# Optimization experiments

Measured on AMD Instinct MI355X. Metric: run time of the kernel, lower is better.

The kernel has to match this reference:

```python
import jax, jax.numpy as jnp
import numpy as np

# ---- static config (mirrors GaussianLSS __init__) ----
ORF_H, ORF_W = 256, 704
FC, FH, FW = 128, 32, 88
D_ST, D_END, D_STEP = 4.0, 45.0, 1.0
OUT_C = 128
ERROR_TOL = 1.0
OPACITY_THR = 0.05
XB = (-50.0, 50.0, 1.0)
YB = (-50.0, 50.0, 1.0)
BEV_H = int(round((YB[1] - YB[0]) / YB[2]))
BEV_W = int(round((XB[1] - XB[0]) / XB[2]))
DS = np.arange(D_ST, D_END, D_STEP, dtype=np.float32)
D = DS.shape[0]  # 41
BN_EPS = 1e-3
CHUNK = 512      # gaussians composited per scan step (16896 = 33*512)
B, NCAM = 1, 6


def make_frustum():
    ds = jnp.broadcast_to(jnp.asarray(DS)[:, None, None], (D, FH, FW))
    xs = jnp.broadcast_to(jnp.linspace(0.0, ORF_W - 1.0, FW)[None, None, :], (D, FH, FW))
    ys = jnp.broadcast_to(jnp.linspace(0.0, ORF_H - 1.0, FH)[None, :, None], (D, FH, FW))
    return jnp.stack([xs, ys, ds], -1)  # [D,FH,FW,3]


def get_geometry(rots, trans, intrins, post_rots, post_trans):
    fr = make_frustum()
    pts = fr[None, None] - post_trans[:, :, None, None, None, :]
    pts = jnp.einsum('bnij,bndhwj->bndhwi', jnp.linalg.inv(post_rots), pts)
    pts = jnp.concatenate([pts[..., :2] * pts[..., 2:3], pts[..., 2:3]], -1)
    comb = jnp.einsum('bnij,bnjk->bnik', rots, jnp.linalg.inv(intrins))
    pts = jnp.einsum('bnij,bndhwj->bndhwi', comb, pts) + trans[:, :, None, None, None, :]
    return pts  # [B,N,D,FH,FW,3] ego-frame frustum points


def conv2d(x, w, b, pad):
    y = jax.lax.conv_general_dilated(x, w, (1, 1), [(pad, pad), (pad, pad)],
                                     dimension_numbers=('NCHW', 'OIHW', 'NCHW'))
    return y + b[None, :, None, None]


def bnorm(x, g, bt, m, v):
    s = (g / jnp.sqrt(v + BN_EPS))[None, :, None, None]
    return (x - m[None, :, None, None]) * s + bt[None, :, None, None]


def splat(means, cov6, colors, ops, valid_in):
    # Differentiable BEV gaussian rasterization (3DGS math, orthographic BEV camera,
    # all depths equal -> compositing in stable gaussian-index order).
    H, W = BEV_H, BEV_W
    sh, sw = H / 2.0, W / 2.0  # h/h_meters with FoV=2 (BEVCamera)
    my = -sh * means[:, 1] + H / 2.0  # pixel row (full_proj_transform row 0)
    mx = -sw * means[:, 0] + W / 2.0  # pixel col (row 1)
    a = sh * sh * cov6[:, 3] + 0.3    # 2D cov = J Sigma_xy J^T, +0.3 low-pass as in 3DGS
    c = sw * sw * cov6[:, 0] + 0.3
    b = sh * sw * cov6[:, 1]
    det = a * c - b * b
    valid = valid_in & (det > 0)
    inv_det = jnp.where(det > 0, 1.0 / det, 0.0)
    cA, cB, cC = c * inv_det, -b * inv_det, a * inv_det
    pi = jnp.repeat(jnp.arange(H, dtype=jnp.float32), W)  # [P] pixel rows
    pj = jnp.tile(jnp.arange(W, dtype=jnp.float32), H)    # [P] pixel cols
    G = means.shape[0]
    nchunk = G // CHUNK
    resh = lambda x: x.reshape((nchunk, CHUNK) + x.shape[1:])
    chunks = (resh(my), resh(mx), resh(cA), resh(cB), resh(cC),
              resh(ops), resh(valid), resh(colors))

    def body(carry, ch):
        logT, acc = carry
        my_c, mx_c, A, Bc, Cc, op_c, val_c, col_c = ch
        dI = pi[None, :] - my_c[:, None]                     # [Gc,P]
        dJ = pj[None, :] - mx_c[:, None]
        q = A[:, None] * dI * dI + 2.0 * Bc[:, None] * dI * dJ + Cc[:, None] * dJ * dJ
        alpha = jnp.minimum(0.99, op_c[:, None] * jnp.exp(-0.5 * q))
        alpha = jnp.where(val_c[:, None] & (q >= 0) & (alpha >= 1.0 / 255.0), alpha, 0.0)
        log1m = jnp.log1p(-alpha)
        cum = jnp.cumsum(log1m, axis=0)
        T = jnp.exp(logT[None, :] + cum - log1m)             # transmittance before each gaussian
        acc = acc + jnp.einsum('gp,gc->pc', alpha * T, col_c)
        return (logT + cum[-1], acc), None

    P = H * W
    init = (jnp.zeros((P,), jnp.float32), jnp.zeros((P, colors.shape[1]), jnp.float32))
    (_, acc), _ = jax.lax.scan(jax.checkpoint(body), init, chunks)
    return acc.reshape(H, W, -1).transpose(2, 0, 1)  # [C,H,W], bg is zeros


def _forward(cam2ego_rot, cam2ego_trans, cam_intrins, post_cam2ego_rot, post_cam2ego_trans,
             img_feats, conv1_w, conv1_b, bn1_g, bn1_b, bn1_m, bn1_v,
             conv2_w, conv2_b, bn2_g, bn2_b, bn2_m, bn2_v, conv3_w, conv3_b):
    geom = get_geometry(cam2ego_rot, cam2ego_trans, cam_intrins, post_cam2ego_rot, post_cam2ego_trans)
    b, n = img_feats.shape[:2]
    x = img_feats.reshape(b * n, FC, FH, FW)
    x = jax.nn.relu(bnorm(conv2d(x, conv1_w, conv1_b, 1), bn1_g, bn1_b, bn1_m, bn1_v))
    x = jax.nn.relu(bnorm(conv2d(x, conv2_w, conv2_b, 1), bn2_g, bn2_b, bn2_m, bn2_v))
    x = conv2d(x, conv3_w, conv3_b, 0)
    depth_prob = jax.nn.softmax(x[:, :D], axis=1).reshape(b, n, D, FH, FW)
    opac = jax.nn.sigmoid(x[:, D:D + 1]).reshape(b, n, FH, FW)
    feats = x[:, D + 1:].reshape(b, n, OUT_C, FH, FW)
    # per-pixel gaussian moments of the depth distribution (compute_gaussian)
    means = jnp.einsum('bndhw,bndhwi->bnhwi', depth_prob, geom)
    delta = means[:, :, None] - geom                                       # [B,N,D,FH,FW,3]
    cov = jnp.einsum('bndhw,bndhwi,bndhwj->bnhwij', depth_prob, delta, delta) * (ERROR_TOL ** 2 / 9.0)
    center = jnp.array([(XB[0] + XB[1]) / 2.0, (YB[0] + YB[1]) / 2.0, 0.0], jnp.float32)
    scale = jnp.array([2.0 / (XB[1] - XB[0]), 2.0 / (YB[1] - YB[0]), 1.0], jnp.float32)
    m_n = (means - center) * scale
    cov_n = cov * (scale[:, None] * scale[None, :])
    cov6 = jnp.stack([cov_n[..., 0, 0], cov_n[..., 0, 1], cov_n[..., 0, 2],
                      cov_n[..., 1, 1], cov_n[..., 1, 2], cov_n[..., 2, 2]], -1)
    g = n * FH * FW
    colors = feats.transpose(0, 1, 3, 4, 2).reshape(b, g, OUT_C)
    m_n = m_n.reshape(b, g, 3)
    cov6 = cov6.reshape(b, g, 6)
    ops = opac.reshape(b, g)
    mask = ops > OPACITY_THR  # opacity filtering == zero contribution, order preserved
    bev = jax.vmap(splat)(m_n, cov6, colors, ops, mask)                    # [B,C,H,W]
    num_gaussians = mask.astype(jnp.float32).sum(-1).mean()
    return bev, num_gaussians


def setup_inputs():
    key = jax.random.key(0)
    ks = jax.random.split(key, 8)
    # camera-to-ego rotations: cam->ego axis permutation composed with per-camera yaw
    yaw = np.linspace(0.0, 2.0 * np.pi, NCAM, endpoint=False).astype(np.float32)
    cz, sz = np.cos(yaw), np.sin(yaw)
    rotz = np.zeros((NCAM, 3, 3), np.float32)
    rotz[:, 0, 0] = cz; rotz[:, 0, 1] = -sz
    rotz[:, 1, 0] = sz; rotz[:, 1, 1] = cz
    rotz[:, 2, 2] = 1.0
    perm = np.array([[0.0, 0.0, 1.0], [-1.0, 0.0, 0.0], [0.0, -1.0, 0.0]], np.float32)
    rots = np.einsum('nij,jk->nik', rotz, perm)
    cam2ego_rot = jnp.asarray(np.broadcast_to(rots, (B, NCAM, 3, 3)).copy())
    cam2ego_trans = jax.random.normal(ks[0], (B, NCAM, 3), jnp.float32)
    K = np.array([[600.0, 0.0, ORF_W / 2.0], [0.0, 600.0, ORF_H / 2.0], [0.0, 0.0, 1.0]], np.float32)
    cam_intrins = jnp.asarray(np.broadcast_to(K, (B, NCAM, 3, 3)).copy())
    post_cam2ego_rot = jnp.broadcast_to(jnp.eye(3, dtype=jnp.float32), (B, NCAM, 3, 3)) + jnp.zeros((B, NCAM, 3, 3), jnp.float32)
    post_cam2ego_trans = jnp.zeros((B, NCAM, 3), jnp.float32)
    img_feats = jax.random.normal(ks[1], (B, NCAM, FC, FH, FW), jnp.float32)
    def conv_init(k, o, i, kh, kw):
        return jax.random.normal(k, (o, i, kh, kw), jnp.float32) * (1.0 / np.sqrt(i * kh * kw))
    return dict(cam2ego_rot=cam2ego_rot, cam2ego_trans=cam2ego_trans, cam_intrins=cam_intrins,
                post_cam2ego_rot=post_cam2ego_rot, post_cam2ego_trans=post_cam2ego_trans,
                img_feats=img_feats,
                conv1_w=conv_init(ks[2], FC, FC, 3, 3), conv1_b=jnp.zeros((FC,), jnp.float32),
                bn1_g=jnp.ones((FC,), jnp.float32), bn1_b=jnp.zeros((FC,), jnp.float32),
                bn1_m=jnp.zeros((FC,), jnp.float32), bn1_v=jnp.ones((FC,), jnp.float32),
                conv2_w=conv_init(ks[3], FC, FC, 3, 3), conv2_b=jnp.zeros((FC,), jnp.float32),
                bn2_g=jnp.ones((FC,), jnp.float32), bn2_b=jnp.zeros((FC,), jnp.float32),
                bn2_m=jnp.zeros((FC,), jnp.float32), bn2_v=jnp.ones((FC,), jnp.float32),
                conv3_w=conv_init(ks[4], OUT_C + D + 1, FC, 1, 1),
                conv3_b=jax.random.normal(ks[5], (OUT_C + D + 1,), jnp.float32) * 0.1)


def reference(cam2ego_rot, cam2ego_trans, cam_intrins, post_cam2ego_rot, post_cam2ego_trans,
              img_feats, conv1_w, conv1_b, bn1_g, bn1_b, bn1_m, bn1_v,
              conv2_w, conv2_b, bn2_g, bn2_b, bn2_m, bn2_v, conv3_w, conv3_b):
    return _forward(cam2ego_rot, cam2ego_trans, cam_intrins, post_cam2ego_rot, post_cam2ego_trans,
                    img_feats, conv1_w, conv1_b, bn1_g, bn1_b, bn1_m, bn1_v,
                    conv2_w, conv2_b, bn2_g, bn2_b, bn2_m, bn2_v, conv3_w, conv3_b)
```

## Files before the change

### kernel.cpp

```cpp
#include <hip/hip_runtime.h>

#define NCAM 6
#define FC   128
#define FH_  32
#define FW_  88
#define NPIX (FH_*FW_)
#define PH   34
#define PW   92
#define PPIX (PH*PW)
#define ND   41
#define X3D  42
#define OUTC 128
#define GTOT (NCAM*NPIX)
#define BEVH 100
#define BEVW 100
#define NPXB (BEVH*BEVW)
#define NTILE 25
#define NWORD 264
#define NMASKW (NTILE*NTILE*NWORD)
#define WCAP  70000
#define CSIZE 64
#define CBLK  2048

#define SZA     (NCAM*FC*PPIX)
#define WS_CAM  0
#define WS_A    256
#define WS_RB   (WS_A  + SZA)
#define WS_X3   (WS_RB + SZA)
#define WS_GS   (WS_X3 + NCAM*X3D*NPIX)
#define WS_WL   (WS_GS + GTOT*8)
#define WS_BASE (WS_WL + WCAP)

__device__ inline void inv3x3(const float* m, float* o) {
    float a=m[0],b=m[1],c=m[2],d=m[3],e=m[4],f=m[5],g=m[6],h=m[7],i=m[8];
    float A=e*i-f*h, B=c*h-b*i, C=b*f-c*e;
    float Dd=f*g-d*i, E=a*i-c*g, F=c*d-a*f;
    float Gg=d*h-e*g, H=b*g-a*h, I=a*e-b*d;
    float r = 1.0f/(a*A + b*Dd + c*Gg);
    o[0]=A*r; o[1]=B*r; o[2]=C*r; o[3]=Dd*r; o[4]=E*r; o[5]=F*r;
    o[6]=Gg*r; o[7]=H*r; o[8]=I*r;
}

__global__ __launch_bounds__(256) void pad_input_kernel(const float* __restrict__ src,
        float* __restrict__ dst, float* __restrict__ rb,
        float* __restrict__ outp, unsigned long long* __restrict__ masks) {
    int idx = blockIdx.x*256 + threadIdx.x;
    if (idx < NMASKW) masks[idx] = 0ull;
    if (idx <= NPXB*OUTC) outp[idx] = 0.0f;
    if (idx >= NCAM*FC*PPIX) return;
    int plane = idx / PPIX, pp = idx - plane*PPIX;
    int y = pp / PW, x = pp - y*PW;
    bool interior = (y >= 1 && y <= FH_ && x >= 1 && x <= FW_);
    float v = 0.0f;
    if (interior)
        v = src[(size_t)plane*NPIX + (y-1)*FW_ + (x-1)];
    dst[idx] = v;
    if (!interior) rb[idx] = 0.0f;
}

__global__ __launch_bounds__(128) void conv3x3_pf_kernel(
        const float* __restrict__ in, float* __restrict__ out, const float* __restrict__ w,
        const float* __restrict__ cb, const float* __restrict__ bg, const float* __restrict__ bb,
        const float* __restrict__ bm, const float* __restrict__ bv) {
    const int n   = blockIdx.x;
    const int co0 = blockIdx.y * 4;
    const int qid = blockIdx.z * 128 + threadIdx.x;
    if (qid >= 704) return;
    const int y = qid / 22, x0 = (qid - y*22) * 4;
    float scale[4], shift[4];
    #pragma unroll
    for (int c=0;c<4;c++) {
        float s = bg[co0+c] * rsqrtf(bv[co0+c] + 1e-3f);
        scale[c] = s;
        shift[c] = (cb[co0+c] - bm[co0+c]) * s + bb[co0+c];
    }
    float acc[4][4] = {};
    const float* ip = in + (size_t)n*FC*PPIX + y*PW + x0;
    const float* wb = w + (size_t)co0*FC*9;
    float4 p4[3]; float2 p2[3];
    #pragma unroll
    for (int r=0;r<3;r++) {
        p4[r] = *(const float4*)(ip + r*PW);
        p2[r] = *(const float2*)(ip + r*PW + 4);
    }
    for (int ci=0; ci<FC; ++ci) {
        float v[3][6];
        #pragma unroll
        for (int r=0;r<3;r++) {
            v[r][0]=p4[r].x; v[r][1]=p4[r].y; v[r][2]=p4[r].z; v[r][3]=p4[r].w;
            v[r][4]=p2[r].x; v[r][5]=p2[r].y;
        }
        if (ci + 1 < FC) {
            const float* ipn = ip + PPIX;
            #pragma unroll
            for (int r=0;r<3;r++) {
                p4[r] = *(const float4*)(ipn + r*PW);
                p2[r] = *(const float2*)(ipn + r*PW + 4);
            }
        }
        #pragma unroll
        for (int c=0;c<4;c++) {
            const float* wr = wb + (size_t)c*FC*9 + ci*9;
            float w00=wr[0],w01=wr[1],w02=wr[2],w10=wr[3],w11=wr[4],
                  w12=wr[5],w20=wr[6],w21=wr[7],w22=wr[8];
            #pragma unroll
            for (int p=0;p<4;p++) {
                float a = acc[c][p];
                a = fmaf(w00, v[0][p], a); a = fmaf(w01, v[0][p+1], a); a = fmaf(w02, v[0][p+2], a);
                a = fmaf(w10, v[1][p], a); a = fmaf(w11, v[1][p+1], a); a = fmaf(w12, v[1][p+2], a);
                a = fmaf(w20, v[2][p], a); a = fmaf(w21, v[2][p+1], a); a = fmaf(w22, v[2][p+2], a);
                acc[c][p] = a;
            }
        }
        ip += PPIX;
    }
    const int po = (y+1)*PW + (x0+1);
    #pragma unroll
    for (int c=0;c<4;c++) {
        float* op = out + ((size_t)n*FC + co0 + c)*PPIX + po;
        #pragma unroll
        for (int p=0;p<4;p++)
            op[p] = fmaxf(fmaf(acc[c][p], scale[c], shift[c]), 0.0f);
    }
}

__global__ __launch_bounds__(256) void conv1x1_kernel(const float* __restrict__ in,
        float* __restrict__ x3d, float* __restrict__ colors,
        const float* __restrict__ w, const float* __restrict__ b) {
    const int n   = blockIdx.x;
    const int px  = blockIdx.y * 256 + threadIdx.x;
    const int co0 = blockIdx.z * 8;
    const int y   = px / FW_, x = px - y*FW_;
    const int pp  = (y+1)*PW + (x+1);
    const float* wr[8];
    float acc[8];
    #pragma unroll
    for (int k=0;k<8;k++) {
        int co = min(co0 + k, 169);
        wr[k]  = w + (size_t)co*FC;
        acc[k] = b[co];
    }
    const float* ip = in + (size_t)n*FC*PPIX + pp;
    #pragma unroll 4
    for (int ci=0; ci<FC; ++ci) {
        float v = ip[(size_t)ci*PPIX];
        #pragma unroll
        for (int k=0;k<8;k++) acc[k] = fmaf(wr[k][ci], v, acc[k]);
    }
    #pragma unroll
    for (int k=0;k<8;k++) {
        int co = co0 + k;
        if (co < X3D)
            x3d[((size_t)n*X3D + co)*NPIX + px] = acc[k];
        else if (co < 170)
            colors[(((size_t)(n*NPIX + px)) << 7) + (co - X3D)] = acc[k];
    }
}

__global__ __launch_bounds__(256) void moments_masks_kernel(const float* __restrict__ x3,
        const float* __restrict__ rot, const float* __restrict__ tr,
        const float* __restrict__ intr, const float* __restrict__ prot,
        const float* __restrict__ ptr_, float* __restrict__ gauss,
        unsigned long long* __restrict__ masks, float* __restrict__ ng) {
    __shared__ float cc[24];
    const int n = blockIdx.x / 11;
    if (threadIdx.x == 0) {
        float M1[9], Ki[9];
        inv3x3(prot + n*9, M1);
        inv3x3(intr + n*9, Ki);
        const float* R = rot + n*9;
        #pragma unroll
        for (int i=0;i<9;i++) cc[i] = M1[i];
        #pragma unroll
        for (int i=0;i<3;i++) cc[9+i] = ptr_[n*3+i];
        #pragma unroll
        for (int i=0;i<3;i++)
            #pragma unroll
            for (int j=0;j<3;j++)
                cc[12+i*3+j] = R[i*3+0]*Ki[0+j] + R[i*3+1]*Ki[3+j] + R[i*3+2]*Ki[6+j];
        #pragma unroll
        for (int i=0;i<3;i++) cc[21+i] = tr[n*3+i];
    }
    __syncthreads();
    const int gi = blockIdx.x*256 + threadIdx.x;
    const int p  = gi - n*NPIX;
    const int h  = p / FW_, xp = p - h*FW_;
    float u = xp * (703.0f/87.0f);
    float v = h  * (255.0f/31.0f);
    float fx = u - cc[9], fy = v - cc[10], fz = -cc[11];
    float p0x = cc[0]*fx + cc[1]*fy + cc[2]*fz;
    float p0y = cc[3]*fx + cc[4]*fy + cc[5]*fz;
    float p0z = cc[6]*fx + cc[7]*fy + cc[8]*fz;
    const float* lg = x3 + (size_t)n*X3D*NPIX + p;

    float lgv[ND];
    #pragma unroll
    for (int d=0; d<ND; ++d) lgv[d] = lg[(size_t)d*NPIX];

    float mxl = -1e30f;
    #pragma unroll
    for (int d=0; d<ND; ++d) mxl = fmaxf(mxl, lgv[d]);

    float s=0.f, sgx=0.f, sgy=0.f;
    #pragma unroll
    for (int d=0; d<ND; ++d) {
        float e  = __expf(lgv[d] - mxl);
        lgv[d] = e;
        float dz = 4.0f + (float)d;
        float pz = p0z + dz*cc[8];
        float px = (p0x + dz*cc[2]) * pz;
        float py = (p0y + dz*cc[5]) * pz;
        float gx = cc[12]*px + cc[13]*py + cc[14]*pz + cc[21];
        float gy = cc[15]*px + cc[16]*py + cc[17]*pz + cc[22];
        s += e; sgx += e*gx; sgy += e*gy;
    }
    float inv_s = 1.0f/s;
    float mex = sgx*inv_s, mey = sgy*inv_s;
    float cxx=0.f, cxy=0.f, cyy=0.f;
    #pragma unroll
    for (int d=0; d<ND; ++d) {
        float e  = lgv[d];
        float dz = 4.0f + (float)d;
        float pz = p0z + dz*cc[8];
        float px = (p0x + dz*cc[2]) * pz;
        float py = (p0y + dz*cc[5]) * pz;
        float gx = cc[12]*px + cc[13]*py + cc[14]*pz + cc[21];
        float gy = cc[15]*px + cc[16]*py + cc[17]*pz + cc[22];
        float dxv = gx - mex, dyv = gy - mey;
        cxx += e*dxv*dxv; cxy += e*dxv*dyv; cyy += e*dyv*dyv;
    }
    const float k9 = inv_s * (1.0f/9.0f);
    cxx *= k9; cxy *= k9; cyy *= k9;

    float lo = lg[(size_t)ND*NPIX];
    float op = 1.0f/(1.0f + __expf(-lo));
    bool mask = op > 0.05f;

    const float SC = 0.02f, SH = 50.0f, SW = 50.0f;
    float my = -SH*(mey*SC) + 50.0f;
    float mx = -SW*(mex*SC) + 50.0f;
    float a  = SH*SH*(cyy*SC*SC) + 0.3f;
    float b  = SH*SW*(cxy*SC*SC);
    float c  = SW*SW*(cxx*SC*SC) + 0.3f;
    float det = a*c - b*b;
    bool valid = mask && (det > 0.0f);
    float A, B2, C, qm, ri, rj;
    if (valid) {
        float idet = 1.0f/det;
        A = c*idet; B2 = -2.0f*b*idet; C = a*idet;
        qm = 2.0f*__logf(255.0f*op);
        ri = sqrtf(qm*a); rj = sqrtf(qm*c);
    } else { A=B2=C=0.f; qm=-1.0f; ri=-1e30f; rj=-1e30f; }
    float* gp = gauss + (size_t)gi*8;
    gp[0]=my; gp[1]=mx; gp[2]=A; gp[3]=B2; gp[4]=C; gp[5]=qm; gp[6]=ri; gp[7]=rj;

    unsigned long long bal = __ballot(mask);
    if ((threadIdx.x & 63) == 0) atomicAdd(ng, (float)__popcll(bal));

    if (!valid) return;
    const float B = 0.5f*B2;
    const float invC = 1.0f / C;
    const float k2 = C*A - B*B;
    int ti0 = max(0, (int)floorf((my - ri) * 0.25f));
    int ti1 = min(NTILE-1, (int)floorf((my + ri) * 0.25f));
    const int wi = gi >> 6;
    const unsigned long long bit = 1ull << (gi & 63);
    for (int ti = ti0; ti <= ti1; ++ti) {
        float jmn = 1e30f, jmx = -1e30f;
        #pragma unroll
        for (int r = 0; r < 4; ++r) {
            int i = 4*ti + r;
            if (i < 0 || i > 99) continue;
            float di = (float)i - my;
            float disc = C*qm - k2*di*di;
            if (disc < 0.0f) continue;
            float sd = sqrtf(disc);
            float jc = -B*di;
            jmn = fminf(jmn, (jc - sd)*invC + mx);
            jmx = fmaxf(jmx, (jc + sd)*invC + mx);
        }
        if (jmx < jmn) continue;
        int jl = max(0, (int)ceilf(jmn));
        int jh = min(99, (int)floorf(jmx));
        if (jl > jh) continue;
        for (int tj = (jl >> 2); tj <= (jh >> 2); ++tj)
            atomicOr(&masks[(size_t)(ti*NTILE + tj)*NWORD + wi], bit);
    }
}

__global__ __launch_bounds__(256) void cnt_kernel(const unsigned long long* __restrict__ masks,
                                                  int* __restrict__ cnt) {
    __shared__ int sc;
    const int tile = blockIdx.x, t = threadIdx.x;
    if (t == 0) sc = 0;
    __syncthreads();
    if (t < NWORD) atomicAdd(&sc, __popcll(masks[(size_t)tile*NWORD + t]));
    __syncthreads();
    if (t == 0) cnt[tile] = sc;
}

__global__ __launch_bounds__(640) void scan_kernel(const int* __restrict__ cnt,
        int* __restrict__ off, int* __restrict__ choff, int* __restrict__ nwork) {
    __shared__ int wsum[16], wsum2[16];
    const int t = threadIdx.x;
    const int lane = t & 63, wv = t >> 6;
    int c  = (t < NTILE*NTILE) ? cnt[t] : 0;
    int ch = (c + CSIZE-1) >> 6;
    int v = c, v2 = ch;
    #pragma unroll
    for (int o = 1; o < 64; o <<= 1) {
        int u  = __shfl_up(v,  (unsigned)o, 64);
        int u2 = __shfl_up(v2, (unsigned)o, 64);
        if (lane >= o) { v += u; v2 += u2; }
    }
    if (lane == 63) { wsum[wv] = v; wsum2[wv] = v2; }
    __syncthreads();
    int pre = 0, pre2 = 0;
    for (int w2 = 0; w2 < wv; ++w2) { pre += wsum[w2]; pre2 += wsum2[w2]; }
    int inc = v + pre, inc2 = v2 + pre2;
    if (t < NTILE*NTILE) { off[t] = inc - c; choff[t] = inc2 - ch; }
    if (t == NTILE*NTILE - 1) {
        off[NTILE*NTILE] = inc;
        choff[NTILE*NTILE] = inc2;
        nwork[0] = (inc2 > WCAP) ? WCAP : inc2;
    }
}

__global__ __launch_bounds__(256) void fill_kernel(const unsigned long long* __restrict__ masks,
        const int* __restrict__ cnt, const int* __restrict__ off, const int* __restrict__ choff,
        unsigned short* __restrict__ list, int* __restrict__ wl) {
    __shared__ unsigned long long sw[NWORD];
    __shared__ int wpre[NWORD];
    const int tile = blockIdx.x, t = threadIdx.x;
    if (t < NWORD) sw[t] = masks[(size_t)tile*NWORD + t];
    __syncthreads();
    if (t == 0) {
        int run = 0;
        for (int w2 = 0; w2 < NWORD; ++w2) { wpre[w2] = run; run += __popcll(sw[w2]); }
    }
    __syncthreads();
    if (t < NWORD) {
        unsigned long long m = sw[t];
        int pos = off[tile] + wpre[t], base = t << 6;
        while (m) { int b = __builtin_ctzll(m); m &= m - 1; list[pos++] = (unsigned short)(base + b); }
    }
    int nch = (cnt[tile] + CSIZE-1)/CSIZE;
    int c0 = choff[tile];
    if (t < nch && c0 + t < WCAP) wl[c0 + t] = (tile << 9) | t;
}

__device__ inline float eval_alpha(const float4 g0, const float4 g1, float fi, float fj) {
    float dI = fi - g0.x, dJ = fj - g0.y;
    float q = dI*(g0.z*dI + g0.w*dJ) + g1.x*dJ*dJ;
    if (q < 0.0f || q > g1.y) return 0.0f;
    return fminf(0.99f, 0.003921568627f * __expf(0.5f*(g1.y - q)));
}

__global__ __launch_bounds__(256) void chunk_sums_kernel(const float* __restrict__ gauss,
        const unsigned short* __restrict__ list, const int* __restrict__ cnt,
        const int* __restrict__ off, const int* __restrict__ wl, const int* __restrict__ nwork,
        float* __restrict__ base) {
    const int nw = nwork[0];
    const int lane = threadIdx.x & 63;
    const int wid  = (blockIdx.x * 256 + threadIdx.x) >> 6;
    const int nwv  = (gridDim.x * 256) >> 6;
    const int px = lane & 15, kg = lane >> 4;
    for (int e = wid; e < nw; e += nwv) {
        int v = wl[e], tile = v >> 9, c = v & 511;
        int hbase = off[tile] + (c << 6);
        int nh = min(CSIZE, cnt[tile] - (c << 6));
        const int i0 = (tile / NTILE) * 4, j0 = (tile % NTILE) * 4;
        const float fi = (float)(i0 + (px >> 2)), fj = (float)(j0 + (px & 3));
        float s = 1.0f;
        for (int k = kg; k < nh; k += 4) {
            int g = list[hbase + k];
            float4 g0 = *(const float4*)(gauss + ((size_t)g << 3));
            float4 g1 = *(const float4*)(gauss + ((size_t)g << 3) + 4);
            float a = eval_alpha(g0, g1, fi, fj);
            s *= (1.0f - a);
        }
        s *= __shfl_xor(s, 16, 64);
        s *= __shfl_xor(s, 32, 64);
        if (lane < 16) base[(size_t)e*16 + lane] = s;
    }
}

__global__ __launch_bounds__(256) void chunk_prefix_kernel(const int* __restrict__ choff,
                                                           float* __restrict__ base) {
    __shared__ float part[16][17];
    const int tile = blockIdx.x, t = threadIdx.x;
    const int c0 = choff[tile], nch = choff[tile+1] - c0;
    if (nch == 0) return;
    const int px = t & 15, cg = t >> 4;
    const int L16 = (nch + 15) >> 4;
    const int a0 = cg*L16, a1 = min(nch, a0 + L16);
    float s = 1.0f;
    for (int c = a0; c < a1; ++c) s *= base[(size_t)(c0 + c)*16 + px];
    part[cg][px] = s;
    __syncthreads();
    if (t < 16) {
        float run = 1.0f;
        #pragma unroll
        for (int k = 0; k < 16; ++k) { float tmp = part[k][t]; part[k][t] = run; run *= tmp; }
    }
    __syncthreads();
    float run = part[cg][px];
    for (int c = a0; c < a1; ++c) {
        size_t idx = (size_t)(c0 + c)*16 + px;
        float tmp = base[idx];
        base[idx] = run;
        run *= tmp;
    }
}

__global__ __launch_bounds__(256) void composite_kernel(const float* __restrict__ gauss,
        const float* __restrict__ colors, const unsigned short* __restrict__ list,
        const int* __restrict__ cnt, const int* __restrict__ off, const int* __restrict__ wl,
        const int* __restrict__ nwork, const float* __restrict__ base, float* __restrict__ out) {
    const int nw = nwork[0];
    const int t = threadIdx.x;
    const int lane = t & 63;
    const int e_px = t >> 4, e_kg = t & 15;
    const int cs4 = t & 31;
    const int par = (t >> 5) & 1;
    const int pq  = t >> 6;
    const int f_pxq = t >> 5;
    const int f_r0  = f_pxq >> 2, f_j = f_pxq & 3;
    __shared__ unsigned short slist[2][CSIZE];
    __shared__ float s_w[CSIZE][17];
    __shared__ float fred[128*17];
    const int per = (nw + CBLK - 1) / CBLK;
    int e0 = blockIdx.x * per;
    if (e0 >= nw) return;
    int e1 = min(nw, e0 + per);

    float4 acc[4];
    #pragma unroll
    for (int j=0;j<4;j++) acc[j] = make_float4(0.f,0.f,0.f,0.f);
    int cur_tile = wl[e0] >> 9;
    int cur_i0 = (cur_tile / NTILE) * 4, cur_j0 = (cur_tile % NTILE) * 4;

    int buf = 0;
    {
        int v = wl[e0], tl = v >> 9, c = v & 511;
        int nh0 = min(CSIZE, cnt[tl] - (c << 6));
        if (t < nh0) slist[0][t] = list[off[tl] + (c << 6) + t];
    }

    for (int e = e0; e < e1; ++e) {
        int v = wl[e], tile = v >> 9, c = v & 511;
        const bool tflush = (tile != cur_tile);
        const int fi0 = cur_i0, fj0 = cur_j0;
        if (tflush) {
            #pragma unroll
            for (int j = 0; j < 4; ++j) {
                acc[j].x += __shfl_xor(acc[j].x, 32, 64);
                acc[j].y += __shfl_xor(acc[j].y, 32, 64);
                acc[j].z += __shfl_xor(acc[j].z, 32, 64);
                acc[j].w += __shfl_xor(acc[j].w, 32, 64);
            }
            if (par == 0) {
                float* fr = &fred[(pq*32 + cs4)*17];
                #pragma unroll
                for (int j = 0; j < 4; ++j) {
                    fr[(j<<2)+0] = acc[j].x; fr[(j<<2)+1] = acc[j].y;
                    fr[(j<<2)+2] = acc[j].z; fr[(j<<2)+3] = acc[j].w;
                }
            }
            #pragma unroll
            for (int j=0;j<4;j++) acc[j] = make_float4(0.f,0.f,0.f,0.f);
            cur_tile = tile;
            cur_i0 = (tile / NTILE) * 4; cur_j0 = (tile % NTILE) * 4;
        }
        const int nh = min(CSIZE, cnt[tile] - (c << 6));
        __syncthreads();
        if (tflush) {
            const float* f0 = &fred[(f_r0*32 + cs4)*17 + (f_j<<2)];
            const float* f1 = &fred[((f_r0+2)*32 + cs4)*17 + (f_j<<2)];
            const int pix0 = (fi0 + f_r0) * BEVW + fj0 + f_j;
            const int pix1 = pix0 + 2 * BEVW;
            float* op = out + (size_t)(cs4 << 2) * NPXB;
            atomicAdd(op + 0*NPXB + pix0, f0[0]); atomicAdd(op + 1*NPXB + pix0, f0[1]);
            atomicAdd(op + 2*NPXB + pix0, f0[2]); atomicAdd(op + 3*NPXB + pix0, f0[3]);
            atomicAdd(op + 0*NPXB + pix1, f1[0]); atomicAdd(op + 1*NPXB + pix1, f1[1]);
            atomicAdd(op + 2*NPXB + pix1, f1[2]); atomicAdd(op + 3*NPXB + pix1, f1[3]);
        }
        if (e + 1 < e1) {
            int v2 = wl[e+1], tl2 = v2 >> 9, c2 = v2 & 511;
            int nh2 = min(CSIZE, cnt[tl2] - (c2 << 6));
            if (t < nh2) slist[buf^1][t] = list[off[tl2] + (c2 << 6) + t];
        }
        {
            const float fi = (float)(cur_i0 + (e_px >> 2)), fj = (float)(cur_j0 + (e_px & 3));
            const int k0 = e_kg << 2;
            float a4[4]; float p = 1.0f;
            #pragma unroll
            for (int i = 0; i < 4; ++i) {
                int k = k0 + i;
                float a = 0.0f;
                if (k < nh) {
                    int g = slist[buf][k];
                    float4 g0 = *(const float4*)(gauss + ((size_t)g << 3));
                    float4 g1 = *(const float4*)(gauss + ((size_t)g << 3) + 4);
                    a = eval_alpha(g0, g1, fi, fj);
                }
                a4[i] = a;
                p *= (1.0f - a);
            }
            float s = p;
            #pragma unroll
            for (int o = 1; o < 16; o <<= 1) {
                float u = __shfl_up(s, (unsigned)o, 64);
                if ((lane & 15) >= o) s *= u;
            }
            float ex = __shfl_up(s, 1u, 64);
            float T = base[(size_t)e*16 + e_px] * (((lane & 15) == 0) ? 1.0f : ex);
            #pragma unroll
            for (int i = 0; i < 4; ++i) {
                float wv = a4[i] * T; T -= wv;
                s_w[k0 + i][e_px] = wv;
            }
        }
        __syncthreads();
        if (nh == CSIZE) {
            #pragma unroll 8
            for (int k = 0; k < CSIZE/2; ++k) {
                const int idx = (k << 1) | par;
                int g = slist[buf][idx];
                const float* swr = s_w[idx] + (pq << 2);
                float w0 = swr[0], w1 = swr[1], w2 = swr[2], w3 = swr[3];
                float4 cl = *(const float4*)(colors + ((size_t)g << 7) + (cs4 << 2));
                acc[0].x = fmaf(w0, cl.x, acc[0].x); acc[0].y = fmaf(w0, cl.y, acc[0].y);
                acc[0].z = fmaf(w0, cl.z, acc[0].z); acc[0].w = fmaf(w0, cl.w, acc[0].w);
                acc[1].x = fmaf(w1, cl.x, acc[1].x); acc[1].y = fmaf(w1, cl.y, acc[1].y);
                acc[1].z = fmaf(w1, cl.z, acc[1].z); acc[1].w = fmaf(w1, cl.w, acc[1].w);
                acc[2].x = fmaf(w2, cl.x, acc[2].x); acc[2].y = fmaf(w2, cl.y, acc[2].y);
                acc[2].z = fmaf(w2, cl.z, acc[2].z); acc[2].w = fmaf(w2, cl.w, acc[2].w);
                acc[3].x = fmaf(w3, cl.x, acc[3].x); acc[3].y = fmaf(w3, cl.y, acc[3].y);
                acc[3].z = fmaf(w3, cl.z, acc[3].z); acc[3].w = fmaf(w3, cl.w, acc[3].w);
            }
        } else {
            #pragma unroll 4
            for (int k = 0; k < CSIZE/2; ++k) {
                const int idx = (k << 1) | par;
                if (idx >= nh) break;
                int g = slist[buf][idx];
                const float* swr = s_w[idx] + (pq << 2);
                float w0 = swr[0], w1 = swr[1], w2 = swr[2], w3 = swr[3];
                float4 cl = *(const float4*)(colors + ((size_t)g << 7) + (cs4 << 2));
                acc[0].x = fmaf(w0, cl.x, acc[0].x); acc[0].y = fmaf(w0, cl.y, acc[0].y);
                acc[0].z = fmaf(w0, cl.z, acc[0].z); acc[0].w = fmaf(w0, cl.w, acc[0].w);
                acc[1].x = fmaf(w1, cl.x, acc[1].x); acc[1].y = fmaf(w1, cl.y, acc[1].y);
                acc[1].z = fmaf(w1, cl.z, acc[1].z); acc[1].w = fmaf(w1, cl.w, acc[1].w);
                acc[2].x = fmaf(w2, cl.x, acc[2].x); acc[2].y = fmaf(w2, cl.y, acc[2].y);
                acc[2].z = fmaf(w2, cl.z, acc[2].z); acc[2].w = fmaf(w2, cl.w, acc[2].w);
                acc[3].x = fmaf(w3, cl.x, acc[3].x); acc[3].y = fmaf(w3, cl.y, acc[3].y);
                acc[3].z = fmaf(w3, cl.z, acc[3].z); acc[3].w = fmaf(w3, cl.w, acc[3].w);
            }
        }
        buf ^= 1;
    }
    #pragma unroll
    for (int j = 0; j < 4; ++j) {
        acc[j].x += __shfl_xor(acc[j].x, 32, 64);
        acc[j].y += __shfl_xor(acc[j].y, 32, 64);
        acc[j].z += __shfl_xor(acc[j].z, 32, 64);
        acc[j].w += __shfl_xor(acc[j].w, 32, 64);
    }
    if (par == 0) {
        float* fr = &fred[(pq*32 + cs4)*17];
        #pragma unroll
        for (int j = 0; j < 4; ++j) {
            fr[(j<<2)+0] = acc[j].x; fr[(j<<2)+1] = acc[j].y;
            fr[(j<<2)+2] = acc[j].z; fr[(j<<2)+3] = acc[j].w;
        }
    }
    __syncthreads();
    {
        const float* f0 = &fred[(f_r0*32 + cs4)*17 + (f_j<<2)];
        const float* f1 = &fred[((f_r0+2)*32 + cs4)*17 + (f_j<<2)];
        const int pix0 = (cur_i0 + f_r0) * BEVW + cur_j0 + f_j;
        const int pix1 = pix0 + 2 * BEVW;
        float* op = out + (size_t)(cs4 << 2) * NPXB;
        atomicAdd(op + 0*NPXB + pix0, f0[0]); atomicAdd(op + 1*NPXB + pix0, f0[1]);
        atomicAdd(op + 2*NPXB + pix0, f0[2]); atomicAdd(op + 3*NPXB + pix0, f0[3]);
        atomicAdd(op + 0*NPXB + pix1, f1[0]); atomicAdd(op + 1*NPXB + pix1, f1[1]);
        atomicAdd(op + 2*NPXB + pix1, f1[2]); atomicAdd(op + 3*NPXB + pix1, f1[3]);
    }
}

extern "C" void kernel_launch(void* const* d_in, const int* in_sizes, int n_in,
                              void* d_out, int out_size, void* d_ws, size_t ws_size,
                              hipStream_t stream) {
    const float* rot  = (const float*)d_in[0];
    const float* tr   = (const float*)d_in[1];
    const float* intr = (const float*)d_in[2];
    const float* prot = (const float*)d_in[3];
    const float* ptr_ = (const float*)d_in[4];
    const float* img  = (const float*)d_in[5];
    const float* c1w  = (const float*)d_in[6];  const float* c1b = (const float*)d_in[7];
    const float* b1g  = (const float*)d_in[8];  const float* b1b = (const float*)d_in[9];
    const float* b1m  = (const float*)d_in[10]; const float* b1v = (const float*)d_in[11];
    const float* c2w  = (const float*)d_in[12]; const float* c2b = (const float*)d_in[13];
    const float* b2g  = (const float*)d_in[14]; const float* b2b = (const float*)d_in[15];
    const float* b2m  = (const float*)d_in[16]; const float* b2v = (const float*)d_in[17];
    const float* c3w  = (const float*)d_in[18]; const float* c3b = (const float*)d_in[19];
    float* out = (float*)d_out;
    float* ws  = (float*)d_ws;
    float* RA  = ws + WS_A;
    float* RB  = ws + WS_RB;
    float* X3B = ws + WS_X3;
    float* GS  = ws + WS_GS;
    int*   WL  = (int*)(ws + WS_WL);
    float* BASE = ws + WS_BASE;
    unsigned long long* MASKS = (unsigned long long*)BASE;
    int* AUXI = (int*)(ws + WS_X3 + 330000);
    int* CNT = AUXI;
    int* OFF = AUXI + 640;
    int* CHOFF = AUXI + 1280;
    int* NWORK = AUXI + 1920;
    unsigned short* LIST = (unsigned short*)RA;
    float* COL = RB;
    float* ngp = out + (size_t)NPXB*OUTC;

    pad_input_kernel<<<(NCAM*FC*PPIX + 255)/256, 256, 0, stream>>>(img, RA, RB, out, MASKS);
    conv3x3_pf_kernel<<<dim3(NCAM,32,6), 128, 0, stream>>>(RA, RB, c1w, c1b, b1g, b1b, b1m, b1v);
    conv3x3_pf_kernel<<<dim3(NCAM,32,6), 128, 0, stream>>>(RB, RA, c2w, c2b, b2g, b2b, b2m, b2v);
    conv1x1_kernel<<<dim3(NCAM,11,22), 256, 0, stream>>>(RA, X3B, COL, c3w, c3b);
    moments_masks_kernel<<<GTOT/256, 256, 0, stream>>>(X3B, rot, tr, intr, prot, ptr_,
                                                       GS, MASKS, ngp);
    cnt_kernel<<<NTILE*NTILE, 256, 0, stream>>>(MASKS, CNT);
    scan_kernel<<<1, 640, 0, stream>>>(CNT, OFF, CHOFF, NWORK);
    fill_kernel<<<NTILE*NTILE, 256, 0, stream>>>(MASKS, CNT, OFF, CHOFF, LIST, WL);
    chunk_sums_kernel<<<8192, 256, 0, stream>>>(GS, LIST, CNT, OFF, WL, NWORK, BASE);
    chunk_prefix_kernel<<<NTILE*NTILE, 256, 0, stream>>>(CHOFF, BASE);
    composite_kernel<<<CBLK, 256, 0, stream>>>(GS, COL, LIST, CNT, OFF, WL, NWORK, BASE, out);
}
```

Baseline: 469.8 us.

## Split moments and tile-mask scatter into separate kernels with 4 threads per gaussian

```diff
diff --git a/kernel.cpp b/kernel.cpp
--- a/kernel.cpp
+++ b/kernel.cpp
@@ -129,39 +129,56 @@
         const float* __restrict__ w, const float* __restrict__ b) {
     const int n   = blockIdx.x;
     const int px  = blockIdx.y * 256 + threadIdx.x;
-    const int co0 = blockIdx.z * 8;
     const int y   = px / FW_, x = px - y*FW_;
     const int pp  = (y+1)*PW + (x+1);
-    const float* wr[8];
-    float acc[8];
-    #pragma unroll
-    for (int k=0;k<8;k++) {
-        int co = min(co0 + k, 169);
-        wr[k]  = w + (size_t)co*FC;
-        acc[k] = b[co];
-    }
     const float* ip = in + (size_t)n*FC*PPIX + pp;
-    #pragma unroll 4
-    for (int ci=0; ci<FC; ++ci) {
-        float v = ip[(size_t)ci*PPIX];
-        #pragma unroll
-        for (int k=0;k<8;k++) acc[k] = fmaf(wr[k][ci], v, acc[k]);
-    }
-    #pragma unroll
-    for (int k=0;k<8;k++) {
-        int co = co0 + k;
-        if (co < X3D)
-            x3d[((size_t)n*X3D + co)*NPIX + px] = acc[k];
-        else if (co < 170)
-            colors[(((size_t)(n*NPIX + px)) << 7) + (co - X3D)] = acc[k];
-    }
-}
-
-__global__ __launch_bounds__(256) void moments_masks_kernel(const float* __restrict__ x3,
+    if (blockIdx.z < 6) {
+        const int co0 = blockIdx.z * 7;
+        const float* wr[7];
+        float acc[7];
+        #pragma unroll
+        for (int k=0;k<7;k++) {
+            int co = co0 + k;
+            wr[k]  = w + (size_t)co*FC;
+            acc[k] = b[co];
+        }
+        #pragma unroll 4
+        for (int ci=0; ci<FC; ++ci) {
+            float v = ip[(size_t)ci*PPIX];
+            #pragma unroll
+            for (int k=0;k<7;k++) acc[k] = fmaf(wr[k][ci], v, acc[k]);
+        }
+        #pragma unroll
+        for (int k=0;k<7;k++)
+            x3d[((size_t)n*X3D + co0 + k)*NPIX + px] = acc[k];
+    } else {
+        const int c0  = (blockIdx.z - 6) * 8;
+        const int co0 = X3D + c0;
+        const float* wr[8];
+        float acc[8];
+        #pragma unroll
+        for (int k=0;k<8;k++) {
+            int co = co0 + k;
+            wr[k]  = w + (size_t)co*FC;
+            acc[k] = b[co];
+        }
+        #pragma unroll 4
+        for (int ci=0; ci<FC; ++ci) {
+            float v = ip[(size_t)ci*PPIX];
+            #pragma unroll
+            for (int k=0;k<8;k++) acc[k] = fmaf(wr[k][ci], v, acc[k]);
+        }
+        float* cp = colors + (((size_t)(n*NPIX + px)) << 7) + c0;
+        *(float4*)(cp)     = make_float4(acc[0], acc[1], acc[2], acc[3]);
+        *(float4*)(cp + 4) = make_float4(acc[4], acc[5], acc[6], acc[7]);
+    }
+}
+
+__global__ __launch_bounds__(256) void moments_kernel(const float* __restrict__ x3,
         const float* __restrict__ rot, const float* __restrict__ tr,
         const float* __restrict__ intr, const float* __restrict__ prot,
         const float* __restrict__ ptr_, float* __restrict__ gauss,
-        unsigned long long* __restrict__ masks, float* __restrict__ ng) {
+        float* __restrict__ ng) {
     __shared__ float cc[24];
     const int n = blockIdx.x / 11;
     if (threadIdx.x == 0) {
@@ -256,16 +273,26 @@
 
     unsigned long long bal = __ballot(mask);
     if ((threadIdx.x & 63) == 0) atomicAdd(ng, (float)__popcll(bal));
-
-    if (!valid) return;
-    const float B = 0.5f*B2;
+}
+
+__global__ __launch_bounds__(256) void scatter_masks_kernel(const float* __restrict__ gauss,
+        unsigned long long* __restrict__ masks) {
+    const int idx = blockIdx.x*256 + threadIdx.x;
+    const int g = idx >> 2, q = idx & 3;
+    const float4 g0 = *(const float4*)(gauss + ((size_t)g << 3));
+    const float4 g1 = *(const float4*)(gauss + ((size_t)g << 3) + 4);
+    if (g1.y < 0.0f) return;
+    const float my = g0.x, mx = g0.y, A = g0.z, B = 0.5f*g0.w, C = g1.x, qm = g1.y, ri = g1.z;
     const float invC = 1.0f / C;
     const float k2 = C*A - B*B;
     int ti0 = max(0, (int)floorf((my - ri) * 0.25f));
     int ti1 = min(NTILE-1, (int)floorf((my + ri) * 0.25f));
-    const int wi = gi >> 6;
-    const unsigned long long bit = 1ull << (gi & 63);
-    for (int ti = ti0; ti <= ti1; ++ti) {
+    int len = ti1 - ti0 + 1;
+    int ta = ti0 + (len*q) / 4;
+    int tb = ti0 + (len*(q+1)) / 4;
+    const int wi = g >> 6;
+    const unsigned long long bit = 1ull << (g & 63);
+    for (int ti = ta; ti < tb; ++ti) {
         float jmn = 1e30f, jmx = -1e30f;
         #pragma unroll
         for (int r = 0; r < 4; ++r) {
@@ -627,8 +654,8 @@
     conv3x3_pf_kernel<<<dim3(NCAM,32,6), 128, 0, stream>>>(RA, RB, c1w, c1b, b1g, b1b, b1m, b1v);
     conv3x3_pf_kernel<<<dim3(NCAM,32,6), 128, 0, stream>>>(RB, RA, c2w, c2b, b2g, b2b, b2m, b2v);
     conv1x1_kernel<<<dim3(NCAM,11,22), 256, 0, stream>>>(RA, X3B, COL, c3w, c3b);
-    moments_masks_kernel<<<GTOT/256, 256, 0, stream>>>(X3B, rot, tr, intr, prot, ptr_,
-                                                       GS, MASKS, ngp);
+    moments_kernel<<<GTOT/256, 256, 0, stream>>>(X3B, rot, tr, intr, prot, ptr_, GS, ngp);
+    scatter_masks_kernel<<<GTOT*4/256, 256, 0, stream>>>(GS, MASKS);
     cnt_kernel<<<NTILE*NTILE, 256, 0, stream>>>(MASKS, CNT);
     scan_kernel<<<1, 640, 0, stream>>>(CNT, OFF, CHOFF, NWORK);
     fill_kernel<<<NTILE*NTILE, 256, 0, stream>>>(MASKS, CNT, OFF, CHOFF, LIST, WL);
```

New measurement: 463.6 us. No clear change (-1.3%).
